# Kernel optimization log

Hardware: AMD Instinct MI355X
Metric: run time of the kernel (lower is better)

Reference implementation:

```python
import jax, jax.numpy as jnp
import numpy as np
import math

B, M, N_BASIS = 4096, 128, 512
A, Bnd, DX = -5.0, 5.0, 100
BANDWIDTH = 0.01
INV_SQRT_2PI = 1.0 / math.sqrt(2.0 * math.pi)


def _phi(t):
    return INV_SQRT_2PI * jnp.exp(-0.5 * t * t)


def _trapz_weights(dtype):
    # uniform-grid trapezoid rule weights: h everywhere, h/2 at endpoints
    h = (Bnd - A) / (DX - 1)
    w = jnp.full((DX,), h, dtype=dtype)
    return w.at[0].mul(0.5).at[-1].mul(0.5)


def setup_inputs() -> dict:
    key = jax.random.key(0)
    k1, k2, k3 = jax.random.split(key, 3)
    theta = jax.random.normal(k1, (B, M + 2), dtype=jnp.float32)
    # theta[:,1] must be negative so sigma_sq = -0.5/theta[:,1] > 0
    theta = theta.at[:, 1].set(-jnp.abs(theta[:, 1]) - 0.5)
    mu = jax.random.normal(k2, (N_BASIS,), dtype=jnp.float32)
    sigma = jax.random.uniform(k3, (N_BASIS,), dtype=jnp.float32) + 0.5
    return {"theta": theta, "mu": mu, "sigma": sigma}


def reference(theta, mu, sigma):
    dt = theta.dtype
    T = jnp.linspace(A, Bnd, DX, dtype=dt)                      # [DX]
    m = theta.shape[1] - 2
    loc = jnp.linspace(0.0, 1.0, m, dtype=dt)                   # [M]
    # gaussian RBF kernel of cdist(loc, T)
    d = loc[:, None] - T[None, :]                               # [M,DX]
    K = jnp.exp(-0.5 * d * d / BANDWIDTH)

    alpha = theta[:, 2:]                                        # [B,M]
    f = alpha @ K                                               # [B,DX]

    sigma_sq = -0.5 / theta[:, 1]                               # [B]
    mu_c = theta[:, 0] * sigma_sq                               # [B]

    # phi1[n, t] = N((mu_n - t)/sigma_n) / sigma_n
    phi1 = _phi((mu[:, None] - T[None, :]) / sigma[:, None]) / sigma[:, None]  # [N,DX]

    # beta_exp(f - 0.5*(mu - T)^2 / sigma_sq), clamped
    quad = 0.5 * (mu_c[:, None] - T[None, :]) ** 2 / sigma_sq[:, None]         # [B,DX]
    exp_terms = jnp.clip(jax.nn.relu(1.0 + f - quad), 1e-8, None)              # [B,DX]

    w = _trapz_weights(dt)                                      # [DX]
    Z = exp_terms @ w                                           # [B]  (trapz over T)
    # trapz_t(phi1 * exp_terms / Z) = ((exp_terms/Z) * w) @ phi1.T
    density = (exp_terms / Z[:, None]) * w[None, :]             # [B,DX]
    return density @ phi1.T                                     # [B,N]
```

## Files before the change

kernel.cpp:

```cpp
#include <hip/hip_runtime.h>
#include <hip/hip_bf16.h>
#include <math.h>

#define NB    512
#define DXN   100
#define MROW  128
#define TC    130
#define G     16
#define BT    512
#define KP    128
#define AP    136
#define T0f   (-5.0f)
#define Hf    (10.0f / 99.0f)
#define LOG2E 1.4426950408889634f
#define WLO   42

typedef __attribute__((ext_vector_type(8))) short  short8;
typedef __attribute__((ext_vector_type(4))) float  f32x4;

__device__ __forceinline__ float Tval(int t) { return T0f + Hf * (float)t; }

__device__ __forceinline__ unsigned short f2bf(float x) {
    __hip_bfloat16 b = __float2bfloat16(x);
    unsigned short u; __builtin_memcpy(&u, &b, 2); return u;
}
__device__ __forceinline__ float bf2f(unsigned short h) {
    return __uint_as_float(((unsigned)h) << 16);
}
__device__ __forceinline__ unsigned pk2bf(float lo, float hi) {
    __hip_bfloat162 b2 = __float22bfloat162_rn(float2{lo, hi});
    unsigned u; __builtin_memcpy(&u, &b2, 4); return u;
}

__global__ __launch_bounds__(BT) void fused_kernel(
    const float* __restrict__ theta,
    const float* __restrict__ mu,
    const float* __restrict__ sigma,
    float* __restrict__ out, int Bn)
{
    __shared__ __align__(16) unsigned short sB[NB * AP];
    __shared__ __align__(16) unsigned short sAlH[G * AP];
    __shared__ __align__(16) unsigned short sAlL[G * AP];
    __shared__ __align__(16) unsigned short sAh[G * AP];
    __shared__ __align__(16) unsigned short sAl[G * AP];
    __shared__ float s_f[G * 32];
    __shared__ __align__(16) float s_muc[G];
    __shared__ __align__(16) float s_negth1[G];
    __shared__ __align__(16) float s_invZ[G];

    const int tid  = threadIdx.x;
    const int b0   = blockIdx.x * G;
    const int lane = tid & 63;
    const int wv   = tid >> 6;
    const int lrow = lane & 15;
    const int kg   = (lane >> 4) * 8;

    const float mun = mu[tid];
    const float sgn = sigma[tid];
    float tv[5];
    #pragma unroll
    for (int k = 0; k < 5; ++k) {
        int i = tid + k * BT;
        int r = i / TC, c = i - r * TC;
        int br = b0 + r; if (br >= Bn) br = Bn - 1;
        tv[k] = (i < G * TC) ? theta[br * TC + c] : 0.0f;
    }

    {
        const float inv_s = 1.0f / sgn;
        const float dlt = Hf * inv_s;
        const float Lh  = 0.5f * LOG2E;
        const float cc  = -2.0f * Lh * dlt * dlt;
        const float S   = __log2f(0.3989422804014327f * inv_s);
        unsigned short* myB = &sB[tid * AP];
        #pragma unroll
        for (int k0 = 0; k0 < 96; k0 += 16) {
            float u  = (mun - Tval(k0)) * inv_s;
            float a  = S - Lh * u * u;
            float bb = Lh * dlt * (2.0f * u - dlt);
            unsigned w[8];
            #pragma unroll
            for (int j = 0; j < 8; ++j) {
                float p0 = __builtin_amdgcn_exp2f(a); a += bb; bb += cc;
                float p1 = __builtin_amdgcn_exp2f(a); a += bb; bb += cc;
                w[j] = pk2bf(p0, p1);
            }
            *(uint4*)&myB[k0]     = make_uint4(w[0], w[1], w[2], w[3]);
            *(uint4*)&myB[k0 + 8] = make_uint4(w[4], w[5], w[6], w[7]);
        }
        {
            float u  = (mun - Tval(96)) * inv_s;
            float a  = S - Lh * u * u;
            float bb = Lh * dlt * (2.0f * u - dlt);
            float p0 = __builtin_amdgcn_exp2f(a); a += bb; bb += cc;
            float p1 = __builtin_amdgcn_exp2f(a); a += bb; bb += cc;
            unsigned w0 = pk2bf(p0, p1);
            p0 = __builtin_amdgcn_exp2f(a); a += bb; bb += cc;
            p1 = __builtin_amdgcn_exp2f(a);
            unsigned w1 = pk2bf(p0, p1);
            *(uint4*)&myB[96]  = make_uint4(w0, w1, 0u, 0u);
            *(uint4*)&myB[104] = make_uint4(0u, 0u, 0u, 0u);
            *(uint4*)&myB[112] = make_uint4(0u, 0u, 0u, 0u);
            *(uint4*)&myB[120] = make_uint4(0u, 0u, 0u, 0u);
        }
    }

    #pragma unroll
    for (int k = 0; k < 5; ++k) {
        int i = tid + k * BT;
        if (i < G * TC) {
            int r = i / TC, c = i - r * TC;
            float v = tv[k];
            if (c >= 2) {
                unsigned short h = f2bf(v);
                sAlH[r * AP + (c - 2)] = h;
                sAlL[r * AP + (c - 2)] = f2bf(v - bf2f(h));
            } else if (c == 0) s_muc[r] = v;
            else               s_negth1[r] = v;
        }
    }
    __syncthreads();

    if (tid < G) {
        float th1 = s_negth1[tid];
        s_muc[tid]    = s_muc[tid] * (-0.5f / th1);
        s_negth1[tid] = -th1;
    }

    if (wv < 2) {
        const int tcol = WLO + wv * 16 + lrow;
        const float T  = Tval(tcol);
        const float C2 = 50.0f * LOG2E;
        const float dj = 1.0f / 127.0f;
        f32x4 fa = {0.0f, 0.0f, 0.0f, 0.0f};
        #pragma unroll
        for (int ks = 0; ks < 4; ++ks) {
            short8 ah = *(const short8*)&sAlH[lrow * AP + ks * 32 + kg];
            short8 al = *(const short8*)&sAlL[lrow * AP + ks * 32 + kg];
            short8 kh, kl;
            #pragma unroll
            for (int jj = 0; jj < 8; ++jj) {
                float d  = (float)(ks * 32 + kg + jj) * dj - T;
                float kv = __builtin_amdgcn_exp2f(-C2 * d * d);
                unsigned short h = f2bf(kv);
                kh[jj] = (short)h;
                kl[jj] = (short)f2bf(kv - bf2f(h));
            }
            fa = __builtin_amdgcn_mfma_f32_16x16x32_bf16(ah, kh, fa, 0, 0, 0);
            fa = __builtin_amdgcn_mfma_f32_16x16x32_bf16(al, kh, fa, 0, 0, 0);
            fa = __builtin_amdgcn_mfma_f32_16x16x32_bf16(ah, kl, fa, 0, 0, 0);
        }
        #pragma unroll
        for (int j = 0; j < 4; ++j)
            s_f[((lane >> 4) * 4 + j) * 32 + wv * 16 + lrow] = fa[j];
    }
    __syncthreads();

    #pragma unroll
    for (int rd = 0; rd < 2; ++rd) {
        const int row = rd * 8 + wv;
        const float muc = s_muc[row], nth = s_negth1[row];
        const int t0 = 2 * lane;
        float dw0 = 0.0f, dw1 = 0.0f;
        if (t0 < DXN) {
            unsigned i0 = (unsigned)(t0 - WLO);
            float f0 = (i0 < 32u) ? s_f[row * 32 + i0] : 0.0f;
            float dm0 = muc - Tval(t0);
            float e0 = fmaxf(1.0f + f0 - nth * dm0 * dm0, 1e-8f);
            dw0 = e0 * ((t0 == 0) ? Hf * 0.5f : Hf);
            const int t1 = t0 + 1;
            unsigned i1 = (unsigned)(t1 - WLO);
            float f1 = (i1 < 32u) ? s_f[row * 32 + i1] : 0.0f;
            float dm1 = muc - Tval(t1);
            float e1 = fmaxf(1.0f + f1 - nth * dm1 * dm1, 1e-8f);
            dw1 = e1 * ((t1 == DXN - 1) ? Hf * 0.5f : Hf);
        }
        unsigned short h0 = f2bf(dw0), h1 = f2bf(dw1);
        unsigned short l0 = f2bf(dw0 - bf2f(h0)), l1 = f2bf(dw1 - bf2f(h1));
        ((unsigned*)sAh)[row * (AP / 2) + lane] = ((unsigned)h1 << 16) | h0;
        ((unsigned*)sAl)[row * (AP / 2) + lane] = ((unsigned)l1 << 16) | l0;
    }
    __syncthreads();

    short8 Ah[4], Al[4];
    #pragma unroll
    for (int ks = 0; ks < 4; ++ks) {
        Ah[ks] = *(const short8*)&sAh[lrow * AP + ks * 32 + kg];
        Al[ks] = *(const short8*)&sAl[lrow * AP + ks * 32 + kg];
    }
    f32x4 acc[4];
    #pragma unroll
    for (int ct = 0; ct < 4; ++ct) {
        const int n = wv * 64 + ct * 16 + lrow;
        f32x4 a = {0.0f, 0.0f, 0.0f, 0.0f};
        #pragma unroll
        for (int ks = 0; ks < 4; ++ks) {
            short8 b = *(const short8*)&sB[n * AP + ks * 32 + kg];
            a = __builtin_amdgcn_mfma_f32_16x16x32_bf16(Ah[ks], b, a, 0, 0, 0);
            a = __builtin_amdgcn_mfma_f32_16x16x32_bf16(Al[ks], b, a, 0, 0, 0);
        }
        acc[ct] = a;
    }
    if (wv == 0) {
        short8 ones;
        #pragma unroll
        for (int jj = 0; jj < 8; ++jj) ones[jj] = (short)0x3F80;
        f32x4 az = {0.0f, 0.0f, 0.0f, 0.0f};
        #pragma unroll
        for (int ks = 0; ks < 4; ++ks) {
            az = __builtin_amdgcn_mfma_f32_16x16x32_bf16(Ah[ks], ones, az, 0, 0, 0);
            az = __builtin_amdgcn_mfma_f32_16x16x32_bf16(Al[ks], ones, az, 0, 0, 0);
        }
        if ((lane & 15) == 0) {
            #pragma unroll
            for (int j = 0; j < 4; ++j)
                s_invZ[(lane >> 4) * 4 + j] = 1.0f / az[j];
        }
    }
    __syncthreads();

    f32x4 iz = *(const f32x4*)&s_invZ[(lane >> 4) * 4];
    #pragma unroll
    for (int ct = 0; ct < 4; ++ct) {
        int col = wv * 64 + ct * 16 + lrow;
        #pragma unroll
        for (int j = 0; j < 4; ++j) {
            int row = b0 + (lane >> 4) * 4 + j;
            if (row < Bn) out[row * NB + col] = acc[ct][j] * iz[j];
        }
    }
}

extern "C" void kernel_launch(void* const* d_in, const int* in_sizes, int n_in,
                              void* d_out, int out_size, void* d_ws, size_t ws_size,
                              hipStream_t stream) {
    const float* theta = (const float*)d_in[0];
    const float* mu    = (const float*)d_in[1];
    const float* sigma = (const float*)d_in[2];
    float* outp = (float*)d_out;

    int Bn = in_sizes[0] / TC;
    int grid = (Bn + G - 1) / G;
    fused_kernel<<<grid, BT, 0, stream>>>(theta, mu, sigma, outp, Bn);
}
```

Measured before the change: 13.02 us.

## Split output columns across two blocks and alias shared buffers for occupancy

```diff
diff --git a/kernel.cpp b/kernel.cpp
--- a/kernel.cpp
+++ b/kernel.cpp
@@ -7,9 +7,10 @@
 #define MROW  128
 #define TC    130
 #define G     16
+#define CB    256
 #define BT    512
 #define KP    128
-#define AP    136
+#define AP    132
 #define T0f   (-5.0f)
 #define Hf    (10.0f / 99.0f)
 #define LOG2E 1.4426950408889634f
@@ -32,31 +33,37 @@
     unsigned u; __builtin_memcpy(&u, &b2, 4); return u;
 }
 
-__global__ __launch_bounds__(BT) void fused_kernel(
+__global__ __launch_bounds__(BT, 4) void fused_kernel(
     const float* __restrict__ theta,
     const float* __restrict__ mu,
     const float* __restrict__ sigma,
     float* __restrict__ out, int Bn)
 {
-    __shared__ __align__(16) unsigned short sB[NB * AP];
-    __shared__ __align__(16) unsigned short sAlH[G * AP];
-    __shared__ __align__(16) unsigned short sAlL[G * AP];
-    __shared__ __align__(16) unsigned short sAh[G * AP];
-    __shared__ __align__(16) unsigned short sAl[G * AP];
+    __shared__ __align__(16) unsigned short sB[CB * AP];
+    __shared__ __align__(16) unsigned short sU[2 * G * AP];
     __shared__ float s_f[G * 32];
     __shared__ __align__(16) float s_muc[G];
     __shared__ __align__(16) float s_negth1[G];
     __shared__ __align__(16) float s_invZ[G];
 
+    unsigned short* sAlH = sU;
+    unsigned short* sAlL = sU + G * AP;
+    unsigned short* sAh  = sU;
+    unsigned short* sAl  = sU + G * AP;
+
     const int tid  = threadIdx.x;
-    const int b0   = blockIdx.x * G;
+    const int bid  = blockIdx.x;
+    const int b0   = (bid & 255) * G;
+    const int c0   = (bid >> 8) * CB;
     const int lane = tid & 63;
     const int wv   = tid >> 6;
     const int lrow = lane & 15;
     const int kg   = (lane >> 4) * 8;
 
-    const float mun = mu[tid];
-    const float sgn = sigma[tid];
+    const int   pcol  = tid >> 1;
+    const int   khalf = tid & 1;
+    const float mun = mu[c0 + pcol];
+    const float sgn = sigma[c0 + pcol];
     float tv[5];
     #pragma unroll
     for (int k = 0; k < 5; ++k) {
@@ -72,36 +79,30 @@
         const float Lh  = 0.5f * LOG2E;
         const float cc  = -2.0f * Lh * dlt * dlt;
         const float S   = __log2f(0.3989422804014327f * inv_s);
-        unsigned short* myB = &sB[tid * AP];
-        #pragma unroll
-        for (int k0 = 0; k0 < 96; k0 += 16) {
-            float u  = (mun - Tval(k0)) * inv_s;
-            float a  = S - Lh * u * u;
-            float bb = Lh * dlt * (2.0f * u - dlt);
-            unsigned w[8];
-            #pragma unroll
-            for (int j = 0; j < 8; ++j) {
-                float p0 = __builtin_amdgcn_exp2f(a); a += bb; bb += cc;
-                float p1 = __builtin_amdgcn_exp2f(a); a += bb; bb += cc;
-                w[j] = pk2bf(p0, p1);
+        unsigned short* myB = &sB[pcol * AP + khalf * 64];
+        #pragma unroll
+        for (int s = 0; s < 4; ++s) {
+            const int k0 = khalf * 64 + s * 16;
+            if (k0 >= DXN + 12) {
+                *(uint4*)&myB[s * 16]     = make_uint4(0u, 0u, 0u, 0u);
+                *(uint4*)&myB[s * 16 + 8] = make_uint4(0u, 0u, 0u, 0u);
+            } else {
+                float u  = (mun - Tval(k0)) * inv_s;
+                float a  = S - Lh * u * u;
+                float bb = Lh * dlt * (2.0f * u - dlt);
+                unsigned w[8];
+                #pragma unroll
+                for (int j = 0; j < 8; ++j) {
+                    int k = k0 + 2 * j;
+                    float p0 = __builtin_amdgcn_exp2f(a); a += bb; bb += cc;
+                    float p1 = __builtin_amdgcn_exp2f(a); a += bb; bb += cc;
+                    if (k     >= DXN) p0 = 0.0f;
+                    if (k + 1 >= DXN) p1 = 0.0f;
+                    w[j] = pk2bf(p0, p1);
+                }
+                *(uint4*)&myB[s * 16]     = make_uint4(w[0], w[1], w[2], w[3]);
+                *(uint4*)&myB[s * 16 + 8] = make_uint4(w[4], w[5], w[6], w[7]);
             }
-            *(uint4*)&myB[k0]     = make_uint4(w[0], w[1], w[2], w[3]);
-            *(uint4*)&myB[k0 + 8] = make_uint4(w[4], w[5], w[6], w[7]);
-        }
-        {
-            float u  = (mun - Tval(96)) * inv_s;
-            float a  = S - Lh * u * u;
-            float bb = Lh * dlt * (2.0f * u - dlt);
-            float p0 = __builtin_amdgcn_exp2f(a); a += bb; bb += cc;
-            float p1 = __builtin_amdgcn_exp2f(a); a += bb; bb += cc;
-            unsigned w0 = pk2bf(p0, p1);
-            p0 = __builtin_amdgcn_exp2f(a); a += bb; bb += cc;
-            p1 = __builtin_amdgcn_exp2f(a);
-            unsigned w1 = pk2bf(p0, p1);
-            *(uint4*)&myB[96]  = make_uint4(w0, w1, 0u, 0u);
-            *(uint4*)&myB[104] = make_uint4(0u, 0u, 0u, 0u);
-            *(uint4*)&myB[112] = make_uint4(0u, 0u, 0u, 0u);
-            *(uint4*)&myB[120] = make_uint4(0u, 0u, 0u, 0u);
         }
     }
 
@@ -188,10 +189,10 @@
         Ah[ks] = *(const short8*)&sAh[lrow * AP + ks * 32 + kg];
         Al[ks] = *(const short8*)&sAl[lrow * AP + ks * 32 + kg];
     }
-    f32x4 acc[4];
-    #pragma unroll
-    for (int ct = 0; ct < 4; ++ct) {
-        const int n = wv * 64 + ct * 16 + lrow;
+    f32x4 acc[2];
+    #pragma unroll
+    for (int ct = 0; ct < 2; ++ct) {
+        const int n = wv * 32 + ct * 16 + lrow;
         f32x4 a = {0.0f, 0.0f, 0.0f, 0.0f};
         #pragma unroll
         for (int ks = 0; ks < 4; ++ks) {
@@ -221,8 +222,8 @@
 
     f32x4 iz = *(const f32x4*)&s_invZ[(lane >> 4) * 4];
     #pragma unroll
-    for (int ct = 0; ct < 4; ++ct) {
-        int col = wv * 64 + ct * 16 + lrow;
+    for (int ct = 0; ct < 2; ++ct) {
+        int col = c0 + wv * 32 + ct * 16 + lrow;
         #pragma unroll
         for (int j = 0; j < 4; ++j) {
             int row = b0 + (lane >> 4) * 4 + j;
@@ -240,6 +241,6 @@
     float* outp = (float*)d_out;
 
     int Bn = in_sizes[0] / TC;
-    int grid = (Bn + G - 1) / G;
+    int grid = ((Bn + G - 1) / G) * 2;
     fused_kernel<<<grid, BT, 0, stream>>>(theta, mu, sigma, outp, Bn);
 }
```

Result: slower. 18.26 us (+40.3%).

## Generate basis phi tiles in registers instead of staging them in LDS

Applied to the files above, without the earlier changes.

```diff
diff --git a/kernel.cpp b/kernel.cpp
--- a/kernel.cpp
+++ b/kernel.cpp
@@ -8,11 +8,12 @@
 #define TC    130
 #define G     16
 #define BT    512
-#define KP    128
-#define AP    136
+#define AP    132
 #define T0f   (-5.0f)
 #define Hf    (10.0f / 99.0f)
 #define LOG2E 1.4426950408889634f
+#define LHALF 0.7213475204444817f
+#define L2PHI (-1.3257480647361593f)
 #define WLO   42
 
 typedef __attribute__((ext_vector_type(8))) short  short8;
@@ -26,10 +27,6 @@
 }
 __device__ __forceinline__ float bf2f(unsigned short h) {
     return __uint_as_float(((unsigned)h) << 16);
-}
-__device__ __forceinline__ unsigned pk2bf(float lo, float hi) {
-    __hip_bfloat162 b2 = __float22bfloat162_rn(float2{lo, hi});
-    unsigned u; __builtin_memcpy(&u, &b2, 4); return u;
 }
 
 __global__ __launch_bounds__(BT) void fused_kernel(
@@ -38,15 +35,13 @@
     const float* __restrict__ sigma,
     float* __restrict__ out, int Bn)
 {
-    __shared__ __align__(16) unsigned short sB[NB * AP];
     __shared__ __align__(16) unsigned short sAlH[G * AP];
     __shared__ __align__(16) unsigned short sAlL[G * AP];
-    __shared__ __align__(16) unsigned short sAh[G * AP];
-    __shared__ __align__(16) unsigned short sAl[G * AP];
+    __shared__ __align__(16) unsigned short sDwH[G * AP];
+    __shared__ __align__(16) unsigned short sDwL[G * AP];
     __shared__ float s_f[G * 32];
     __shared__ __align__(16) float s_muc[G];
     __shared__ __align__(16) float s_negth1[G];
-    __shared__ __align__(16) float s_invZ[G];
 
     const int tid  = threadIdx.x;
     const int b0   = blockIdx.x * G;
@@ -54,9 +49,17 @@
     const int wv   = tid >> 6;
     const int lrow = lane & 15;
     const int kg   = (lane >> 4) * 8;
-
-    const float mun = mu[tid];
-    const float sgn = sigma[tid];
+    const float kgf = (float)kg;
+
+    float mun4[4], is4[4], S4[4];
+    #pragma unroll
+    for (int ct = 0; ct < 4; ++ct) {
+        const int n = wv * 64 + ct * 16 + lrow;
+        float m = mu[n], s = sigma[n];
+        mun4[ct] = m;
+        is4[ct]  = __builtin_amdgcn_rcpf(s);
+        S4[ct]   = L2PHI - __log2f(s);
+    }
     float tv[5];
     #pragma unroll
     for (int k = 0; k < 5; ++k) {
@@ -64,45 +67,6 @@
         int r = i / TC, c = i - r * TC;
         int br = b0 + r; if (br >= Bn) br = Bn - 1;
         tv[k] = (i < G * TC) ? theta[br * TC + c] : 0.0f;
-    }
-
-    {
-        const float inv_s = 1.0f / sgn;
-        const float dlt = Hf * inv_s;
-        const float Lh  = 0.5f * LOG2E;
-        const float cc  = -2.0f * Lh * dlt * dlt;
-        const float S   = __log2f(0.3989422804014327f * inv_s);
-        unsigned short* myB = &sB[tid * AP];
-        #pragma unroll
-        for (int k0 = 0; k0 < 96; k0 += 16) {
-            float u  = (mun - Tval(k0)) * inv_s;
-            float a  = S - Lh * u * u;
-            float bb = Lh * dlt * (2.0f * u - dlt);
-            unsigned w[8];
-            #pragma unroll
-            for (int j = 0; j < 8; ++j) {
-                float p0 = __builtin_amdgcn_exp2f(a); a += bb; bb += cc;
-                float p1 = __builtin_amdgcn_exp2f(a); a += bb; bb += cc;
-                w[j] = pk2bf(p0, p1);
-            }
-            *(uint4*)&myB[k0]     = make_uint4(w[0], w[1], w[2], w[3]);
-            *(uint4*)&myB[k0 + 8] = make_uint4(w[4], w[5], w[6], w[7]);
-        }
-        {
-            float u  = (mun - Tval(96)) * inv_s;
-            float a  = S - Lh * u * u;
-            float bb = Lh * dlt * (2.0f * u - dlt);
-            float p0 = __builtin_amdgcn_exp2f(a); a += bb; bb += cc;
-            float p1 = __builtin_amdgcn_exp2f(a); a += bb; bb += cc;
-            unsigned w0 = pk2bf(p0, p1);
-            p0 = __builtin_amdgcn_exp2f(a); a += bb; bb += cc;
-            p1 = __builtin_amdgcn_exp2f(a);
-            unsigned w1 = pk2bf(p0, p1);
-            *(uint4*)&myB[96]  = make_uint4(w0, w1, 0u, 0u);
-            *(uint4*)&myB[104] = make_uint4(0u, 0u, 0u, 0u);
-            *(uint4*)&myB[112] = make_uint4(0u, 0u, 0u, 0u);
-            *(uint4*)&myB[120] = make_uint4(0u, 0u, 0u, 0u);
-        }
     }
 
     #pragma unroll
@@ -126,7 +90,7 @@
         s_muc[tid]    = s_muc[tid] * (-0.5f / th1);
         s_negth1[tid] = -th1;
     }
-
+    short8 bc[2][4];
     if (wv < 2) {
         const int tcol = WLO + wv * 16 + lrow;
         const float T  = Tval(tcol);
@@ -153,6 +117,21 @@
         #pragma unroll
         for (int j = 0; j < 4; ++j)
             s_f[((lane >> 4) * 4 + j) * 32 + wv * 16 + lrow] = fa[j];
+    } else {
+        #pragma unroll
+        for (int ct = 0; ct < 2; ++ct) {
+            #pragma unroll
+            for (int ks = 0; ks < 4; ++ks) {
+                #pragma unroll
+                for (int jj = 0; jj < 8; ++jj) {
+                    int k = ks * 32 + kg + jj;
+                    float u = (mun4[ct] - (T0f + Hf * (float)k)) * is4[ct];
+                    float p = __builtin_amdgcn_exp2f(__builtin_fmaf(-LHALF * u, u, S4[ct]));
+                    if (k >= DXN) p = 0.0f;
+                    bc[ct][ks][jj] = (short)f2bf(p);
+                }
+            }
+        }
     }
     __syncthreads();
 
@@ -177,56 +156,61 @@
         }
         unsigned short h0 = f2bf(dw0), h1 = f2bf(dw1);
         unsigned short l0 = f2bf(dw0 - bf2f(h0)), l1 = f2bf(dw1 - bf2f(h1));
-        ((unsigned*)sAh)[row * (AP / 2) + lane] = ((unsigned)h1 << 16) | h0;
-        ((unsigned*)sAl)[row * (AP / 2) + lane] = ((unsigned)l1 << 16) | l0;
+        ((unsigned*)sDwH)[row * (AP / 2) + lane] = ((unsigned)h1 << 16) | h0;
+        ((unsigned*)sDwL)[row * (AP / 2) + lane] = ((unsigned)l1 << 16) | l0;
     }
     __syncthreads();
 
     short8 Ah[4], Al[4];
     #pragma unroll
     for (int ks = 0; ks < 4; ++ks) {
-        Ah[ks] = *(const short8*)&sAh[lrow * AP + ks * 32 + kg];
-        Al[ks] = *(const short8*)&sAl[lrow * AP + ks * 32 + kg];
-    }
-    f32x4 acc[4];
+        Ah[ks] = *(const short8*)&sDwH[lrow * AP + ks * 32 + kg];
+        Al[ks] = *(const short8*)&sDwL[lrow * AP + ks * 32 + kg];
+    }
+
+    short8 ones;
+    #pragma unroll
+    for (int jj = 0; jj < 8; ++jj) ones[jj] = (short)0x3F80;
+    f32x4 az = {0.0f, 0.0f, 0.0f, 0.0f};
+    #pragma unroll
+    for (int ks = 0; ks < 4; ++ks) {
+        az = __builtin_amdgcn_mfma_f32_16x16x32_bf16(Ah[ks], ones, az, 0, 0, 0);
+        az = __builtin_amdgcn_mfma_f32_16x16x32_bf16(Al[ks], ones, az, 0, 0, 0);
+    }
+    float iz[4];
+    #pragma unroll
+    for (int j = 0; j < 4; ++j) iz[j] = __builtin_amdgcn_rcpf(az[j]);
+
     #pragma unroll
     for (int ct = 0; ct < 4; ++ct) {
-        const int n = wv * 64 + ct * 16 + lrow;
+        short8 bh[4];
+        if (wv >= 2 && ct < 2) {
+            #pragma unroll
+            for (int ks = 0; ks < 4; ++ks) bh[ks] = bc[ct][ks];
+        } else {
+            #pragma unroll
+            for (int ks = 0; ks < 4; ++ks) {
+                #pragma unroll
+                for (int jj = 0; jj < 8; ++jj) {
+                    int k = ks * 32 + kg + jj;
+                    float u = (mun4[ct] - (T0f + Hf * (float)k)) * is4[ct];
+                    float p = __builtin_amdgcn_exp2f(__builtin_fmaf(-LHALF * u, u, S4[ct]));
+                    if (k >= DXN) p = 0.0f;
+                    bh[ks][jj] = (short)f2bf(p);
+                }
+            }
+        }
         f32x4 a = {0.0f, 0.0f, 0.0f, 0.0f};
         #pragma unroll
         for (int ks = 0; ks < 4; ++ks) {
-            short8 b = *(const short8*)&sB[n * AP + ks * 32 + kg];
-            a = __builtin_amdgcn_mfma_f32_16x16x32_bf16(Ah[ks], b, a, 0, 0, 0);
-            a = __builtin_amdgcn_mfma_f32_16x16x32_bf16(Al[ks], b, a, 0, 0, 0);
-        }
-        acc[ct] = a;
-    }
-    if (wv == 0) {
-        short8 ones;
-        #pragma unroll
-        for (int jj = 0; jj < 8; ++jj) ones[jj] = (short)0x3F80;
-        f32x4 az = {0.0f, 0.0f, 0.0f, 0.0f};
-        #pragma unroll
-        for (int ks = 0; ks < 4; ++ks) {
-            az = __builtin_amdgcn_mfma_f32_16x16x32_bf16(Ah[ks], ones, az, 0, 0, 0);
-            az = __builtin_amdgcn_mfma_f32_16x16x32_bf16(Al[ks], ones, az, 0, 0, 0);
-        }
-        if ((lane & 15) == 0) {
-            #pragma unroll
-            for (int j = 0; j < 4; ++j)
-                s_invZ[(lane >> 4) * 4 + j] = 1.0f / az[j];
-        }
-    }
-    __syncthreads();
-
-    f32x4 iz = *(const f32x4*)&s_invZ[(lane >> 4) * 4];
-    #pragma unroll
-    for (int ct = 0; ct < 4; ++ct) {
-        int col = wv * 64 + ct * 16 + lrow;
+            a = __builtin_amdgcn_mfma_f32_16x16x32_bf16(Ah[ks], bh[ks], a, 0, 0, 0);
+            a = __builtin_amdgcn_mfma_f32_16x16x32_bf16(Al[ks], bh[ks], a, 0, 0, 0);
+        }
+        const int col = wv * 64 + ct * 16 + lrow;
         #pragma unroll
         for (int j = 0; j < 4; ++j) {
             int row = b0 + (lane >> 4) * 4 + j;
-            if (row < Bn) out[row * NB + col] = acc[ct][j] * iz[j];
+            if (row < Bn) out[row * NB + col] = a[j] * iz[j];
         }
     }
 }
```

Measured after the change: 15.02 us. +15.4%, slower.

## Split basis columns across two blocks and compute Z redundantly per wave

Applied to the files above, without the earlier changes.

```diff
diff --git a/kernel.cpp b/kernel.cpp
--- a/kernel.cpp
+++ b/kernel.cpp
@@ -7,9 +7,9 @@
 #define MROW  128
 #define TC    130
 #define G     16
-#define BT    512
-#define KP    128
-#define AP    136
+#define CB    256
+#define BT    256
+#define AP    132
 #define T0f   (-5.0f)
 #define Hf    (10.0f / 99.0f)
 #define LOG2E 1.4426950408889634f
@@ -32,34 +32,37 @@
     unsigned u; __builtin_memcpy(&u, &b2, 4); return u;
 }
 
-__global__ __launch_bounds__(BT) void fused_kernel(
+__global__ __launch_bounds__(BT, 2) void fused_kernel(
     const float* __restrict__ theta,
     const float* __restrict__ mu,
     const float* __restrict__ sigma,
     float* __restrict__ out, int Bn)
 {
-    __shared__ __align__(16) unsigned short sB[NB * AP];
-    __shared__ __align__(16) unsigned short sAlH[G * AP];
-    __shared__ __align__(16) unsigned short sAlL[G * AP];
-    __shared__ __align__(16) unsigned short sAh[G * AP];
-    __shared__ __align__(16) unsigned short sAl[G * AP];
+    __shared__ __align__(16) unsigned short sB[CB * AP];
+    __shared__ __align__(16) unsigned short sU[2 * G * AP];
     __shared__ float s_f[G * 32];
     __shared__ __align__(16) float s_muc[G];
     __shared__ __align__(16) float s_negth1[G];
-    __shared__ __align__(16) float s_invZ[G];
+
+    unsigned short* sAlH = sU;
+    unsigned short* sAlL = sU + G * AP;
+    unsigned short* sDwH = sU;
+    unsigned short* sDwL = sU + G * AP;
 
     const int tid  = threadIdx.x;
-    const int b0   = blockIdx.x * G;
+    const int bid  = blockIdx.x;
+    const int b0   = (bid >> 1) * G;
+    const int c0   = (bid & 1) * CB;
     const int lane = tid & 63;
     const int wv   = tid >> 6;
     const int lrow = lane & 15;
     const int kg   = (lane >> 4) * 8;
 
-    const float mun = mu[tid];
-    const float sgn = sigma[tid];
-    float tv[5];
-    #pragma unroll
-    for (int k = 0; k < 5; ++k) {
+    const float mun = mu[c0 + tid];
+    const float sgn = sigma[c0 + tid];
+    float tv[9];
+    #pragma unroll
+    for (int k = 0; k < 9; ++k) {
         int i = tid + k * BT;
         int r = i / TC, c = i - r * TC;
         int br = b0 + r; if (br >= Bn) br = Bn - 1;
@@ -106,7 +109,7 @@
     }
 
     #pragma unroll
-    for (int k = 0; k < 5; ++k) {
+    for (int k = 0; k < 9; ++k) {
         int i = tid + k * BT;
         if (i < G * TC) {
             int r = i / TC, c = i - r * TC;
@@ -126,7 +129,6 @@
         s_muc[tid]    = s_muc[tid] * (-0.5f / th1);
         s_negth1[tid] = -th1;
     }
-
     if (wv < 2) {
         const int tcol = WLO + wv * 16 + lrow;
         const float T  = Tval(tcol);
@@ -157,8 +159,8 @@
     __syncthreads();
 
     #pragma unroll
-    for (int rd = 0; rd < 2; ++rd) {
-        const int row = rd * 8 + wv;
+    for (int rd = 0; rd < 4; ++rd) {
+        const int row = rd * 4 + wv;
         const float muc = s_muc[row], nth = s_negth1[row];
         const int t0 = 2 * lane;
         float dw0 = 0.0f, dw1 = 0.0f;
@@ -177,18 +179,30 @@
         }
         unsigned short h0 = f2bf(dw0), h1 = f2bf(dw1);
         unsigned short l0 = f2bf(dw0 - bf2f(h0)), l1 = f2bf(dw1 - bf2f(h1));
-        ((unsigned*)sAh)[row * (AP / 2) + lane] = ((unsigned)h1 << 16) | h0;
-        ((unsigned*)sAl)[row * (AP / 2) + lane] = ((unsigned)l1 << 16) | l0;
+        ((unsigned*)sDwH)[row * (AP / 2) + lane] = ((unsigned)h1 << 16) | h0;
+        ((unsigned*)sDwL)[row * (AP / 2) + lane] = ((unsigned)l1 << 16) | l0;
     }
     __syncthreads();
 
     short8 Ah[4], Al[4];
     #pragma unroll
     for (int ks = 0; ks < 4; ++ks) {
-        Ah[ks] = *(const short8*)&sAh[lrow * AP + ks * 32 + kg];
-        Al[ks] = *(const short8*)&sAl[lrow * AP + ks * 32 + kg];
-    }
-    f32x4 acc[4];
+        Ah[ks] = *(const short8*)&sDwH[lrow * AP + ks * 32 + kg];
+        Al[ks] = *(const short8*)&sDwL[lrow * AP + ks * 32 + kg];
+    }
+    short8 ones;
+    #pragma unroll
+    for (int jj = 0; jj < 8; ++jj) ones[jj] = (short)0x3F80;
+    f32x4 az = {0.0f, 0.0f, 0.0f, 0.0f};
+    #pragma unroll
+    for (int ks = 0; ks < 4; ++ks) {
+        az = __builtin_amdgcn_mfma_f32_16x16x32_bf16(Ah[ks], ones, az, 0, 0, 0);
+        az = __builtin_amdgcn_mfma_f32_16x16x32_bf16(Al[ks], ones, az, 0, 0, 0);
+    }
+    float iz[4];
+    #pragma unroll
+    for (int j = 0; j < 4; ++j) iz[j] = __builtin_amdgcn_rcpf(az[j]);
+
     #pragma unroll
     for (int ct = 0; ct < 4; ++ct) {
         const int n = wv * 64 + ct * 16 + lrow;
@@ -199,34 +213,11 @@
             a = __builtin_amdgcn_mfma_f32_16x16x32_bf16(Ah[ks], b, a, 0, 0, 0);
             a = __builtin_amdgcn_mfma_f32_16x16x32_bf16(Al[ks], b, a, 0, 0, 0);
         }
-        acc[ct] = a;
-    }
-    if (wv == 0) {
-        short8 ones;
-        #pragma unroll
-        for (int jj = 0; jj < 8; ++jj) ones[jj] = (short)0x3F80;
-        f32x4 az = {0.0f, 0.0f, 0.0f, 0.0f};
-        #pragma unroll
-        for (int ks = 0; ks < 4; ++ks) {
-            az = __builtin_amdgcn_mfma_f32_16x16x32_bf16(Ah[ks], ones, az, 0, 0, 0);
-            az = __builtin_amdgcn_mfma_f32_16x16x32_bf16(Al[ks], ones, az, 0, 0, 0);
-        }
-        if ((lane & 15) == 0) {
-            #pragma unroll
-            for (int j = 0; j < 4; ++j)
-                s_invZ[(lane >> 4) * 4 + j] = 1.0f / az[j];
-        }
-    }
-    __syncthreads();
-
-    f32x4 iz = *(const f32x4*)&s_invZ[(lane >> 4) * 4];
-    #pragma unroll
-    for (int ct = 0; ct < 4; ++ct) {
-        int col = wv * 64 + ct * 16 + lrow;
+        const int col = c0 + n;
         #pragma unroll
         for (int j = 0; j < 4; ++j) {
             int row = b0 + (lane >> 4) * 4 + j;
-            if (row < Bn) out[row * NB + col] = acc[ct][j] * iz[j];
+            if (row < Bn) out[row * NB + col] = a[j] * iz[j];
         }
     }
 }
@@ -240,6 +231,6 @@
     float* outp = (float*)d_out;
 
     int Bn = in_sizes[0] / TC;
-    int grid = (Bn + G - 1) / G;
+    int grid = ((Bn + G - 1) / G) * 2;
     fused_kernel<<<grid, BT, 0, stream>>>(theta, mu, sigma, outp, Bn);
 }
```

Result: slower. 16.94 us (+30.1%).
